# Optimization experiments

Measured on AMD Instinct MI355X. Metric: run time of the kernel, lower is better.

Reference implementation:

```python
import jax, jax.numpy as jnp
import numpy as np

B, L, S, H = 2, 256, 384, 768
Tc, Dc = 16, 50
WV, WD = 20000, 100
CV = 128
NEG = -1e30


def _lstm_scan(x, Wih, Whh, bih, bhh):
    # x: [N, T, D] -> hs: [N, T, Hc]; torch LSTM gate order i,f,g,o
    N = x.shape[0]
    Hc = Whh.shape[1]
    h0 = jnp.zeros((N, Hc), x.dtype)

    def step(carry, xt):
        h, c = carry
        g = xt @ Wih.T + h @ Whh.T + bih + bhh  # [N, 4Hc]
        i, f, gg, o = jnp.split(g, 4, axis=-1)
        i = jax.nn.sigmoid(i)
        f = jax.nn.sigmoid(f)
        gg = jnp.tanh(gg)
        o = jax.nn.sigmoid(o)
        c = f * c + i * gg
        h = o * jnp.tanh(c)
        return (h, c), h

    _, hs = jax.lax.scan(step, (h0, h0), jnp.swapaxes(x, 0, 1))
    return jnp.swapaxes(hs, 0, 1)


def setup_inputs() -> dict:
    key = jax.random.key(0)
    ks = jax.random.split(key, 10)
    bert_emb = jax.random.normal(ks[0], (B, S, H), jnp.float32)
    pieces2word = jax.random.randint(ks[1], (B, L, S), 0, 2, jnp.int32)
    word_ids = jax.random.randint(ks[2], (B, L), 0, WV, jnp.int32)
    char_count = jax.random.randint(ks[3], (B, L), 1, Tc + 1, jnp.int32)
    char_ids = jax.random.randint(ks[4], (B, L, Tc), 0, CV, jnp.int32)
    # mask consistent with ragged char lengths (first char_count positions valid)
    token_masks_char = (jnp.arange(Tc)[None, None, :] < char_count[..., None]).astype(jnp.int32)
    word_table = jax.random.normal(ks[5], (WV, WD), jnp.float32) * 0.02
    char_table = jax.random.normal(ks[6], (CV, Dc), jnp.float32) * 0.02
    sc = 1.0 / np.sqrt(Dc)

    def lstm_w(k):
        a, b, c, d = jax.random.split(k, 4)
        return (jax.random.uniform(a, (4 * Dc, Dc), jnp.float32, -sc, sc),
                jax.random.uniform(b, (4 * Dc, Dc), jnp.float32, -sc, sc),
                jax.random.uniform(c, (4 * Dc,), jnp.float32, -sc, sc),
                jax.random.uniform(d, (4 * Dc,), jnp.float32, -sc, sc))

    Wih_f, Whh_f, bih_f, bhh_f = lstm_w(ks[7])
    Wih_b, Whh_b, bih_b, bhh_b = lstm_w(ks[8])
    return dict(bert_emb=bert_emb, pieces2word=pieces2word, word_ids=word_ids,
                char_count=char_count, char_ids=char_ids, token_masks_char=token_masks_char,
                word_table=word_table, char_table=char_table,
                Wih_f=Wih_f, Whh_f=Whh_f, bih_f=bih_f, bhh_f=bhh_f,
                Wih_b=Wih_b, Whh_b=Whh_b, bih_b=bih_b, bhh_b=bhh_b)


def reference(bert_emb, pieces2word, word_ids, char_count, char_ids, token_masks_char,
              word_table, char_table, Wih_f, Whh_f, bih_f, bhh_f, Wih_b, Whh_b, bih_b, bhh_b):
    # --- piece2word max pool (expand + masked_fill(min) + max over pieces) ---
    minv = jnp.min(bert_emb)
    # [B, L, S, H] intermediate, as in the original expand
    masked = jnp.where(pieces2word[..., None] != 0, bert_emb[:, None, :, :], minv)
    word_reps = jnp.max(masked, axis=2)  # [B, L, H]
    # dropouts are identity in eval mode

    # --- word embedding lookup ---
    word_embed = word_table[word_ids]  # [B, L, WD]

    # --- char bi-LSTM with packed-sequence semantics ---
    lens = jnp.maximum(char_count.reshape(-1), 1)  # char_count[char_count==0]=1
    x = char_table[char_ids.reshape(B * L, Tc)]  # [N, Tc, Dc]
    h_fwd = _lstm_scan(x, Wih_f, Whh_f, bih_f, bhh_f)
    # reverse each sequence within its valid length for the backward direction
    t = jnp.arange(Tc)[None, :]
    idx = jnp.where(t < lens[:, None], lens[:, None] - 1 - t, t)  # [N, Tc]
    x_rev = jnp.take_along_axis(x, idx[..., None], axis=1)
    h_bwd = _lstm_scan(x_rev, Wih_b, Whh_b, bih_b, bhh_b)
    h_bwd = jnp.take_along_axis(h_bwd, idx[..., None], axis=1)  # back to original order
    h = jnp.concatenate([h_fwd, h_bwd], axis=-1)  # [N, Tc, 2*Dc]
    valid = (t < lens[:, None])[..., None]
    h = jnp.where(valid, h, 0.0)  # pad_packed_sequence zero-pads beyond length
    h = h.reshape(B, L, Tc, 2 * Dc)

    # --- combine(..., 'max'): masked max over ragged char groups ---
    m = jnp.where(token_masks_char[..., None] == 0, NEG, 0.0)
    sup = jnp.max(m + h, axis=2)  # [B, L, 2*Dc]
    sup = jnp.where(sup == NEG, 0.0, sup)

    return jnp.concatenate([word_reps, word_embed, sup], axis=-1)  # [B, L, H+WD+2*Dc]
```

## Files before the change

### kernel.cpp

```cpp
#include <hip/hip_runtime.h>
#include <float.h>

#define Bb 2
#define Ll 256
#define Ss 384
#define Hh 768
#define Tc 16
#define Dc 50
#define WD 100
#define CV 128
#define NG 200
#define OUTC 968


__device__ inline float tanh_fast(float x) {
    float e = __expf(2.f * x);
    return 1.f - 2.f / (e + 1.f);
}
__device__ inline float sigmoid_fast(float x) {
    return 1.f / (1.f + __expf(-x));
}


__global__ __launch_bounds__(256) void kernel1(
        const float* __restrict__ bert, const float* __restrict__ char_table,
        const float* __restrict__ Wih_f, const float* __restrict__ bih_f, const float* __restrict__ bhh_f,
        const float* __restrict__ Wih_b, const float* __restrict__ bih_b, const float* __restrict__ bhh_b,
        float* __restrict__ minp, float* __restrict__ xpt) {
    int blk = blockIdx.x, tid = threadIdx.x;
    if (blk < 128) {
        const int n4 = (Bb * Ss * Hh) / 4;
        const float4* b4 = (const float4*)bert;
        float m = FLT_MAX;
        for (int i = blk * 256 + tid; i < n4; i += 128 * 256) {
            float4 v = b4[i];
            m = fminf(m, fminf(fminf(v.x, v.y), fminf(v.z, v.w)));
        }
        #pragma unroll
        for (int off = 32; off; off >>= 1) m = fminf(m, __shfl_down(m, off, 64));
        __shared__ float red[4];
        if ((tid & 63) == 0) red[tid >> 6] = m;
        __syncthreads();
        if (tid == 0) minp[blk] = fminf(fminf(red[0], red[1]), fminf(red[2], red[3]));
    } else {
        int idx = blk - 128;
        int dir = idx >> 3, c0 = (idx & 7) * 16;
        const float* Wih = dir ? Wih_b : Wih_f;
        const float* bih = dir ? bih_b : bih_f;
        const float* bhh = dir ? bhh_b : bhh_f;
        __shared__ float ct[16][Dc];
        for (int e = tid; e < 16 * Dc; e += 256)
            ((float*)ct)[e] = char_table[c0 * Dc + e];
        __syncthreads();
        if (tid < NG) {
            float w[Dc];
            #pragma unroll
            for (int j = 0; j < Dc; j++) w[j] = Wih[tid * Dc + j];
            float bias = bih[tid] + bhh[tid];
            for (int cid = 0; cid < 16; cid++) {
                float a = bias;
                #pragma unroll
                for (int j = 0; j < Dc; j++) a += w[j] * ct[cid][j];
                xpt[(dir * CV + c0 + cid) * NG + tid] = a;
            }
        }
    }
}


__global__ __launch_bounds__(256) void kernel2(
        const int* __restrict__ char_ids, const int* __restrict__ char_count,
        const float* __restrict__ Whh_f, const float* __restrict__ Whh_b,
        const float* __restrict__ xpt,
        const float* __restrict__ bert, const int* __restrict__ p2w,
        const float* __restrict__ minp,
        const int* __restrict__ word_ids, const float* __restrict__ word_table,
        float* __restrict__ out) {
    __shared__ __align__(16) char smem[16392];
    int blk = blockIdx.x, tid = threadIdx.x;

    if (blk < 1024) {
        float (*xg)[NG] = (float (*)[NG])smem;
        float* gs  = (float*)(smem + 12800);
        float* hs  = (float*)(smem + 13600);
        int*   scid = (int*)(smem + 13808);

        int n = blk >> 1, dir = blk & 1;
        const float* Whh = dir ? Whh_b : Whh_f;

        int len = char_count[n];
        if (len < 1) len = 1;
        if (tid < Tc) {
            int t = tid;
            int st = dir ? (t < len ? len - 1 - t : t) : t;
            scid[t] = char_ids[n * Tc + st];
        }
        if (tid < 52) hs[tid] = 0.f;
        __syncthreads();

        for (int e = tid; e < Tc * (NG / 4); e += 256) {
            int t = e / 50, q = e - t * 50;
            ((float4*)xg[t])[q] = ((const float4*)&xpt[(dir * CV + scid[t]) * NG])[q];
        }
        int wrow = tid < NG ? tid : NG - 1;
        bool istanh = (tid >= 100 && tid < 150);
        float w[52];
        #pragma unroll
        for (int j = 0; j < Dc; j++) w[j] = Whh[wrow * Dc + j];
        w[50] = 0.f; w[51] = 0.f;
        __syncthreads();

        float c = 0.f, maxv = -FLT_MAX;
        for (int t = 0; t < Tc; t++) {
            #pragma unroll
            for (int j = 0; j < 52; j++) asm volatile("" : "+v"(w[j]));
            if (tid < NG) {
                float g = xg[t][tid];
                #pragma unroll
                for (int j = 0; j < 52; j += 4) {
                    float4 hv = *(const float4*)&hs[j];
                    g += hv.x * w[j] + hv.y * w[j+1] + hv.z * w[j+2] + hv.w * w[j+3];
                }
                gs[tid] = istanh ? tanh_fast(g) : sigmoid_fast(g);
            }
            __syncthreads();
            if (tid < Dc) {
                float si = gs[tid];
                float sf = gs[tid + 50];
                float tg = gs[tid + 100];
                float so = gs[tid + 150];
                c = sf * c + si * tg;
                float h = so * tanh_fast(c);
                hs[tid] = h;
                if (t < len) maxv = fmaxf(maxv, h);
            }
            __syncthreads();
        }
        if (tid < Dc)
            out[(size_t)n * OUTC + (Hh + WD) + dir * Dc + tid] = maxv;
    } else if (blk < 1408) {
        float (*sacc)[8][128] = (float (*)[8][128])smem;
        float* sminv = (float*)(smem + 16384);

        if (tid < 64) {
            float m = fminf(minp[tid], minp[tid + 64]);
            #pragma unroll
            for (int off = 32; off; off >>= 1) m = fminf(m, __shfl_down(m, off, 64));
            if (tid == 0) *sminv = m;
        }
        int idx = blk - 1024;
        int hc  = idx % 6;
        int lt  = (idx / 6) & 31;
        int b   = idx / 192;
        int l0  = lt * 8;
        int w    = tid >> 6;
        int lane = tid & 63;
        int s0 = w * 96;

        const int* pm = p2w + ((size_t)(b * Ll + l0)) * Ss + s0;
        unsigned m0[8], m1[8], m2[8];
        #pragma unroll
        for (int r = 0; r < 8; r++) {
            unsigned long long b0 = __ballot(pm[r * Ss + lane] != 0);
            unsigned long long b1 = __ballot(lane < 32 ? (pm[r * Ss + 64 + lane] != 0) : false);
            m0[r] = __builtin_amdgcn_readfirstlane((unsigned)b0);
            m1[r] = __builtin_amdgcn_readfirstlane((unsigned)(b0 >> 32));
            m2[r] = __builtin_amdgcn_readfirstlane((unsigned)b1);
        }

        const float2* bb2 = (const float2*)(bert + (size_t)b * Ss * Hh) + hc * 64 + lane;
        float2 acc[8];
        #pragma unroll
        for (int r = 0; r < 8; r++) { acc[r].x = -FLT_MAX; acc[r].y = -FLT_MAX; }

        for (int jo = 0; jo < 96; jo += 8) {
            float2 v[8];
            #pragma unroll
            for (int k = 0; k < 8; k++) v[k] = bb2[(size_t)(s0 + jo + k) * 384];
            #pragma unroll
            for (int k = 0; k < 8; k++) {
                int j = jo + k;
                #pragma unroll
                for (int r = 0; r < 8; r++) {
                    unsigned bit = (j < 32 ? m0[r] >> j
                                 : j < 64 ? m1[r] >> (j - 32)
                                          : m2[r] >> (j - 64)) & 1u;
                    if (bit) {
                        acc[r].x = fmaxf(acc[r].x, v[k].x);
                        acc[r].y = fmaxf(acc[r].y, v[k].y);
                    }
                }
            }
        }
        #pragma unroll
        for (int r = 0; r < 8; r++)
            *(float2*)&sacc[w][r][lane * 2] = acc[r];
        __syncthreads();

        float mv = *sminv;
        for (int e = tid; e < 8 * 128; e += 256) {
            int r = e >> 7, cx = e & 127;
            float m = fmaxf(fmaxf(sacc[0][r][cx], sacc[1][r][cx]),
                            fmaxf(sacc[2][r][cx], sacc[3][r][cx]));
            if (m == -FLT_MAX) m = mv;
            out[((size_t)(b * Ll + l0 + r)) * OUTC + hc * 128 + cx] = m;
        }
    } else {
        for (int i = (blk - 1408) * 256 + tid; i < Bb * Ll * WD; i += 64 * 256) {
            int bl = i / WD, d = i - bl * WD;
            out[(size_t)bl * OUTC + Hh + d] = word_table[(size_t)word_ids[bl] * WD + d];
        }
    }
}

extern "C" void kernel_launch(void* const* d_in, const int* in_sizes, int n_in,
                              void* d_out, int out_size, void* d_ws, size_t ws_size,
                              hipStream_t stream) {
    const float* bert       = (const float*)d_in[0];
    const int*   p2w        = (const int*)d_in[1];
    const int*   word_ids   = (const int*)d_in[2];
    const int*   char_count = (const int*)d_in[3];
    const int*   char_ids   = (const int*)d_in[4];
    const float* word_table = (const float*)d_in[6];
    const float* char_table = (const float*)d_in[7];
    const float* Wih_f = (const float*)d_in[8];
    const float* Whh_f = (const float*)d_in[9];
    const float* bih_f = (const float*)d_in[10];
    const float* bhh_f = (const float*)d_in[11];
    const float* Wih_b = (const float*)d_in[12];
    const float* Whh_b = (const float*)d_in[13];
    const float* bih_b = (const float*)d_in[14];
    const float* bhh_b = (const float*)d_in[15];
    float* out = (float*)d_out;

    float* minp = (float*)d_ws;
    float* xpt  = minp + 128;

    kernel1<<<144, 256, 0, stream>>>(
        bert, char_table, Wih_f, bih_f, bhh_f, Wih_b, bih_b, bhh_b,
        minp, xpt);
    kernel2<<<1472, 256, 0, stream>>>(
        char_ids, char_count, Whh_f, Whh_b, xpt, bert, p2w, minp,
        word_ids, word_table, out);
}
```

Measured before the change: 150.2 us.

## Interleave pooling and LSTM blocks, halve pooling rows, use additive smem mask

After: 123.5 us. -17.8%, faster.

```diff
diff --git a/kernel.cpp b/kernel.cpp
--- a/kernel.cpp
+++ b/kernel.cpp
@@ -68,7 +68,7 @@
 }
 
 
-__global__ __launch_bounds__(256) void kernel2(
+__global__ __launch_bounds__(256, 4) void kernel2(
         const int* __restrict__ char_ids, const int* __restrict__ char_count,
         const float* __restrict__ Whh_f, const float* __restrict__ Whh_b,
         const float* __restrict__ xpt,
@@ -76,24 +76,28 @@
         const float* __restrict__ minp,
         const int* __restrict__ word_ids, const float* __restrict__ word_table,
         float* __restrict__ out) {
-    __shared__ __align__(16) char smem[16392];
+    __shared__ __align__(16) char smem[14592];
     int blk = blockIdx.x, tid = threadIdx.x;
 
-    if (blk < 1024) {
+    int role, id;
+    if (blk < 1536) { role = blk & 1; id = blk >> 1; }
+    else if (blk < 1792) { role = 1; id = 768 + (blk - 1536); }
+    else { role = 2; id = blk - 1792; }
+
+    if (role == 1) {
         float (*xg)[NG] = (float (*)[NG])smem;
         float* gs  = (float*)(smem + 12800);
         float* hs  = (float*)(smem + 13600);
         int*   scid = (int*)(smem + 13808);
 
-        int n = blk >> 1, dir = blk & 1;
+        int n = id >> 1, dir = id & 1;
         const float* Whh = dir ? Whh_b : Whh_f;
 
         int len = char_count[n];
         if (len < 1) len = 1;
         if (tid < Tc) {
-            int t = tid;
-            int st = dir ? (t < len ? len - 1 - t : t) : t;
-            scid[t] = char_ids[n * Tc + st];
+            int st = dir ? (tid < len ? len - 1 - tid : tid) : tid;
+            scid[tid] = char_ids[n * Tc + st];
         }
         if (tid < 52) hs[tid] = 0.f;
         __syncthreads();
@@ -138,40 +142,37 @@
         }
         if (tid < Dc)
             out[(size_t)n * OUTC + (Hh + WD) + dir * Dc + tid] = maxv;
-    } else if (blk < 1408) {
-        float (*sacc)[8][128] = (float (*)[8][128])smem;
-        float* sminv = (float*)(smem + 16384);
-
+    } else if (role == 0) {
+        float (*sm)[4] = (float (*)[4])smem;
+        float (*sacc)[4][128] = (float (*)[4][128])(smem + 6144);
+        float* sminv = (float*)(smem + 14336);
+
+        int hc  = id % 6;
+        int lt  = (id / 6) & 63;
+        int b   = id / 384;
+        int l0  = lt * 4;
+
+        const int* pm = p2w + ((size_t)(b * Ll + l0)) * Ss;
+        for (int e = tid; e < 4 * Ss; e += 256) {
+            int r = e / Ss, s = e - r * Ss;
+            sm[s][r] = pm[r * Ss + s] ? 0.f : -FLT_MAX;
+        }
         if (tid < 64) {
             float m = fminf(minp[tid], minp[tid + 64]);
             #pragma unroll
             for (int off = 32; off; off >>= 1) m = fminf(m, __shfl_down(m, off, 64));
             if (tid == 0) *sminv = m;
         }
-        int idx = blk - 1024;
-        int hc  = idx % 6;
-        int lt  = (idx / 6) & 31;
-        int b   = idx / 192;
-        int l0  = lt * 8;
+        __syncthreads();
+
         int w    = tid >> 6;
         int lane = tid & 63;
         int s0 = w * 96;
 
-        const int* pm = p2w + ((size_t)(b * Ll + l0)) * Ss + s0;
-        unsigned m0[8], m1[8], m2[8];
-        #pragma unroll
-        for (int r = 0; r < 8; r++) {
-            unsigned long long b0 = __ballot(pm[r * Ss + lane] != 0);
-            unsigned long long b1 = __ballot(lane < 32 ? (pm[r * Ss + 64 + lane] != 0) : false);
-            m0[r] = __builtin_amdgcn_readfirstlane((unsigned)b0);
-            m1[r] = __builtin_amdgcn_readfirstlane((unsigned)(b0 >> 32));
-            m2[r] = __builtin_amdgcn_readfirstlane((unsigned)b1);
-        }
-
         const float2* bb2 = (const float2*)(bert + (size_t)b * Ss * Hh) + hc * 64 + lane;
-        float2 acc[8];
-        #pragma unroll
-        for (int r = 0; r < 8; r++) { acc[r].x = -FLT_MAX; acc[r].y = -FLT_MAX; }
+        float2 acc[4];
+        #pragma unroll
+        for (int r = 0; r < 4; r++) { acc[r].x = -FLT_MAX; acc[r].y = -FLT_MAX; }
 
         for (int jo = 0; jo < 96; jo += 8) {
             float2 v[8];
@@ -179,26 +180,25 @@
             for (int k = 0; k < 8; k++) v[k] = bb2[(size_t)(s0 + jo + k) * 384];
             #pragma unroll
             for (int k = 0; k < 8; k++) {
-                int j = jo + k;
-                #pragma unroll
-                for (int r = 0; r < 8; r++) {
-                    unsigned bit = (j < 32 ? m0[r] >> j
-                                 : j < 64 ? m1[r] >> (j - 32)
-                                          : m2[r] >> (j - 64)) & 1u;
-                    if (bit) {
-                        acc[r].x = fmaxf(acc[r].x, v[k].x);
-                        acc[r].y = fmaxf(acc[r].y, v[k].y);
-                    }
-                }
-            }
-        }
-        #pragma unroll
-        for (int r = 0; r < 8; r++)
+                int j = s0 + jo + k;
+                float4 q = *(const float4*)&sm[j][0];
+                acc[0].x = fmaxf(acc[0].x, v[k].x + q.x);
+                acc[0].y = fmaxf(acc[0].y, v[k].y + q.x);
+                acc[1].x = fmaxf(acc[1].x, v[k].x + q.y);
+                acc[1].y = fmaxf(acc[1].y, v[k].y + q.y);
+                acc[2].x = fmaxf(acc[2].x, v[k].x + q.z);
+                acc[2].y = fmaxf(acc[2].y, v[k].y + q.z);
+                acc[3].x = fmaxf(acc[3].x, v[k].x + q.w);
+                acc[3].y = fmaxf(acc[3].y, v[k].y + q.w);
+            }
+        }
+        #pragma unroll
+        for (int r = 0; r < 4; r++)
             *(float2*)&sacc[w][r][lane * 2] = acc[r];
         __syncthreads();
 
         float mv = *sminv;
-        for (int e = tid; e < 8 * 128; e += 256) {
+        for (int e = tid; e < 4 * 128; e += 256) {
             int r = e >> 7, cx = e & 127;
             float m = fmaxf(fmaxf(sacc[0][r][cx], sacc[1][r][cx]),
                             fmaxf(sacc[2][r][cx], sacc[3][r][cx]));
@@ -206,7 +206,7 @@
             out[((size_t)(b * Ll + l0 + r)) * OUTC + hc * 128 + cx] = m;
         }
     } else {
-        for (int i = (blk - 1408) * 256 + tid; i < Bb * Ll * WD; i += 64 * 256) {
+        for (int i = id * 256 + tid; i < Bb * Ll * WD; i += 64 * 256) {
             int bl = i / WD, d = i - bl * WD;
             out[(size_t)bl * OUTC + Hh + d] = word_table[(size_t)word_ids[bl] * WD + d];
         }
@@ -239,7 +239,7 @@
     kernel1<<<144, 256, 0, stream>>>(
         bert, char_table, Wih_f, bih_f, bhh_f, Wih_b, bih_b, bhh_b,
         minp, xpt);
-    kernel2<<<1472, 256, 0, stream>>>(
+    kernel2<<<1856, 256, 0, stream>>>(
         char_ids, char_count, Whh_f, Whh_b, xpt, bert, p2w, minp,
         word_ids, word_table, out);
 }
```
